# Optimization experiments

Hardware: AMD Instinct MI355X
Metric: run time of the kernel (lower is better)

The kernel has to match this reference:

```python
import jax, jax.numpy as jnp
import numpy as np

EPS = 1e-8
LAMBDA_SOFTMAX = 9.0
LAMBDA_LSE = 6.0
MARGIN = 0.2


def setup_inputs() -> dict:
    key = jax.random.key(0)
    k1, k2, k3 = jax.random.split(key, 3)
    B, R, W, D = 128, 36, 64, 1024
    im = jax.random.normal(k1, (B, R, D), dtype=jnp.float32)
    s = jax.random.normal(k2, (B, W, D), dtype=jnp.float32)
    s_l = jax.random.randint(k3, (B,), 8, W + 1, dtype=jnp.int32)
    return {"im": im, "s": s, "s_l": s_l}


def _xattn_scores_t2i(im, s, s_l):
    # im: [B, R, D] images; s: [B, W, D] captions; s_l: [B] caption lengths
    B, W = s.shape[0], s.shape[1]
    wmask = (jnp.arange(W)[None, :] < s_l[:, None]).astype(im.dtype)  # [B, W]

    def per_caption(args):
        cap, wm = args  # cap: [W, D], wm: [W]
        # raw attention: context=images, query=caption words -> [B, R, W]
        attn = jnp.einsum('ird,wd->irw', im, cap)
        # clipped_l2norm: leakyrelu(0.1) then l2norm over word dim; padded words zeroed
        attn = jax.nn.leaky_relu(attn, 0.1) * wm
        attn = attn / (jnp.sqrt(jnp.sum(attn * attn, axis=2, keepdims=True)) + EPS)
        # transpose to [B, W, R], softmax over regions with smoothing
        attn = jax.nn.softmax(jnp.swapaxes(attn, 1, 2) * LAMBDA_SOFTMAX, axis=2)
        # weighted image context per word: [B, W, D]
        wei = jnp.einsum('iwr,ird->iwd', attn, im)
        # cosine similarity between caption words and weighted context
        num = jnp.einsum('iwd,wd->iw', wei, cap)
        n_cap = jnp.sqrt(jnp.sum(cap * cap, axis=-1))      # [W]
        n_wei = jnp.sqrt(jnp.sum(wei * wei, axis=-1))      # [B, W]
        row = num / jnp.maximum(n_cap[None, :] * n_wei, EPS)
        # LogSumExp aggregation over valid words -> [B]
        return jnp.log(jnp.sum(jnp.exp(LAMBDA_LSE * row) * wm[None, :], axis=1)) / LAMBDA_LSE

    cols = jax.lax.map(per_caption, (s, wmask))  # [B_cap, B_img]
    return cols.T  # scores[i, j]: image i vs caption j


def reference(im, s, s_l):
    scores = _xattn_scores_t2i(im, s, s_l)  # [B, B]
    B = scores.shape[0]
    diag = jnp.diagonal(scores)[:, None]  # [B, 1]
    cost_s = jnp.clip(MARGIN + scores - diag, 0.0)       # caption retrieval
    cost_im = jnp.clip(MARGIN + scores - diag.T, 0.0)    # image retrieval
    off = 1.0 - jnp.eye(B, dtype=scores.dtype)
    cost_s = cost_s * off
    cost_im = cost_im * off
    # max_violation=True: hardest negatives
    cost_s = jnp.max(cost_s, axis=1)
    cost_im = jnp.max(cost_im, axis=0)
    return jnp.sum(cost_s) + jnp.sum(cost_im)
```

## Files before the change

### kernel.cpp

```cpp
#include <hip/hip_runtime.h>
#include <hip/hip_bf16.h>
#include <math.h>
#include <stdint.h>

#define NB 128
#define NR 36
#define NW 64
#define ND 1024
#define MT 48
#define EPSF 1e-8f
#define LAM_SM 9.0f
#define LAM_LSE 6.0f
#define MARGINF 0.2f

typedef _Float16 f16;
typedef f16 f16x4 __attribute__((ext_vector_type(4)));
typedef f16 f16x8 __attribute__((ext_vector_type(8)));
typedef float f32x4 __attribute__((ext_vector_type(4)));
typedef int i32x4 __attribute__((ext_vector_type(4)));
typedef int i32x8 __attribute__((ext_vector_type(8)));

__device__ __forceinline__ void gld_lds16(const void* g, void* l) {
    __builtin_amdgcn_global_load_lds(
        (const __attribute__((address_space(1))) uint32_t*)(uintptr_t)g,
        (__attribute__((address_space(3))) uint32_t*)(uint32_t)(uintptr_t)l,
        16, 0, 0);
}

__device__ __forceinline__ uint32_t pk_fp8x4(float4 v) {
    uint32_t w = 0;
    w = __builtin_amdgcn_cvt_pk_fp8_f32(v.x, v.y, w, false);
    w = __builtin_amdgcn_cvt_pk_fp8_f32(v.z, v.w, w, true);
    return w;
}

__global__ __launch_bounds__(256) void prep_kernel(
    const float* __restrict__ im, const float* __restrict__ s,
    uint8_t* __restrict__ im8, uint8_t* __restrict__ s8, float* __restrict__ ncap,
    f16* __restrict__ Mg16) {
    __shared__ __align__(16) char Gs[8192];
    const int b = blockIdx.x, y = blockIdx.y, t = threadIdx.x;

    if (y < 14) {
        const int lr = t >> 5, g = t & 31;
        const int row = y * 8 + lr;
        if (row < MT) {
            uint32_t* dst = (uint32_t*)(im8 + ((size_t)b * MT + row) * ND);
            if (row < NR) {
                const float4* src = (const float4*)(im + ((size_t)b * NR + row) * ND);
                #pragma unroll
                for (int e = 0; e < 8; ++e)
                    dst[g + e * 32] = pk_fp8x4(src[g + e * 32]);
            } else {
                #pragma unroll
                for (int e = 0; e < 8; ++e) dst[g + e * 32] = 0u;
            }
        } else {
            const int w = row - MT;
            const float4* src = (const float4*)(s + ((size_t)b * NW + w) * ND);
            uint32_t* dst = (uint32_t*)(s8 + ((size_t)b * NW + w) * ND);
            float ss = 0.f;
            #pragma unroll
            for (int e = 0; e < 8; ++e) {
                float4 v = src[g + e * 32];
                dst[g + e * 32] = pk_fp8x4(v);
                ss += v.x * v.x + v.y * v.y + v.z * v.z + v.w * v.w;
            }
            #pragma unroll
            for (int off = 1; off < 32; off <<= 1) ss += __shfl_xor(ss, off, 32);
            if (g == 0) ncap[b * NW + w] = sqrtf(ss);
        }
        return;
    }

    const int wave = t >> 6, lane = t & 63;
    const int quad = lane >> 4, l16 = lane & 15;
    const int nt = wave;
    f32x4 acc[3];
    acc[0] = (f32x4){0.f, 0.f, 0.f, 0.f};
    acc[1] = (f32x4){0.f, 0.f, 0.f, 0.f};
    acc[2] = (f32x4){0.f, 0.f, 0.f, 0.f};
    const float* imb = im + (size_t)b * NR * ND;

    for (int kk = 0; kk < ND; kk += 64) {
        for (int cidx = t; cidx < 512; cidx += 256) {
            int row = cidx >> 3, c = cidx & 7;
            f16x8 hv;
            if (row < NR) {
                const float4* sp = (const float4*)(imb + (size_t)row * ND + kk + c * 8);
                float4 v0 = sp[0], v1 = sp[1];
                hv = (f16x8){(f16)v0.x, (f16)v0.y, (f16)v0.z, (f16)v0.w,
                             (f16)v1.x, (f16)v1.y, (f16)v1.z, (f16)v1.w};
            } else {
                hv = (f16x8){(f16)0.f, (f16)0.f, (f16)0.f, (f16)0.f,
                             (f16)0.f, (f16)0.f, (f16)0.f, (f16)0.f};
            }
            *(f16x8*)(Gs + row * 128 + ((c ^ (row & 7)) * 16)) = hv;
        }
        __syncthreads();
        #pragma unroll
        for (int ks = 0; ks < 2; ++ks) {
            int brow = nt * 16 + l16;
            f16x8 bf = *(const f16x8*)(Gs + brow * 128 + (((ks * 4 + quad) ^ (brow & 7)) * 16));
            #pragma unroll
            for (int mt = 0; mt < 3; ++mt) {
                int arow = mt * 16 + l16;
                f16x8 af = *(const f16x8*)(Gs + arow * 128 + (((ks * 4 + quad) ^ (arow & 7)) * 16));
                acc[mt] = __builtin_amdgcn_mfma_f32_16x16x32_f16(af, bf, acc[mt], 0, 0, 0);
            }
        }
        __syncthreads();
    }
    f16* Mb = Mg16 + (size_t)b * (MT * NW);
    #pragma unroll
    for (int mt = 0; mt < 3; ++mt) {
        #pragma unroll
        for (int r = 0; r < 4; ++r) {
            int row = mt * 16 + quad * 4 + r;
            Mb[row * NW + nt * 16 + l16] = (f16)acc[mt][r];
        }
    }
}

#define A_LDS 12288
__global__ __launch_bounds__(256) void fused_pair_kernel(
    const uint8_t* __restrict__ im8, const uint8_t* __restrict__ s8,
    const int* __restrict__ s_l, const f16* __restrict__ Mg16,
    const float* __restrict__ ncap, float* __restrict__ scores) {
    __shared__ __align__(16) char lds[32768];
    const int t = threadIdx.x;
    const int wave = t >> 6, lane = t & 63;
    const int quad = lane >> 4, l16 = lane & 15;
    const int wi = wave >> 1, wj = wave & 1;

    const int lin = blockIdx.x;
    const int gx = lin & 63, gy = lin >> 6;
    const int i = gy * 2 + wi;
    const int j = gx * 2 + wj;
    const int L = s_l[j];

    const uint8_t* Ab = im8 + (size_t)gy * 2 * (MT * ND);
    const uint8_t* Bb = s8 + (size_t)gx * 2 * (NW * ND);

    int goff[7];
    bool gact[7];
    const uint8_t* gbase[7];
    #pragma unroll
    for (int q = 0; q < 7; ++q) {
        int f = q * 4096 + t * 16;
        if (f < A_LDS) {
            int row = f >> 7, c = (f >> 4) & 7;
            goff[q] = row * ND + (c ^ (row & 7)) * 16;
            gact[q] = (row % MT) < NR;
            gbase[q] = Ab;
        } else {
            int f2 = f - A_LDS;
            int row = f2 >> 7, c = (f2 >> 4) & 7;
            goff[q] = row * ND + (c ^ (row & 7)) * 16;
            gact[q] = true;
            gbase[q] = Bb;
        }
    }

    if (t < 192) {
        int r = (t < 96) ? (36 + (t >> 3)) : (84 + ((t - 96) >> 3));
        *(float4*)(lds + r * 128 + (t & 7) * 16) = make_float4(0.f, 0.f, 0.f, 0.f);
    }

    f32x4 acc[3][4];
    #pragma unroll
    for (int mi = 0; mi < 3; ++mi)
        #pragma unroll
        for (int nt = 0; nt < 4; ++nt)
            acc[mi][nt] = (f32x4){0.f, 0.f, 0.f, 0.f};

    const int c0 = quad * 2, c1 = quad * 2 + 1;

    for (int kk = 0; kk < ND; kk += 128) {
        #pragma unroll
        for (int q = 0; q < 7; ++q)
            if (gact[q]) gld_lds16(gbase[q] + goff[q] + kk, lds + q * 4096 + t * 16);
        __syncthreads();
        i32x8 bf[4];
        #pragma unroll
        for (int nt = 0; nt < 4; ++nt) {
            int row = wj * 64 + nt * 16 + l16;
            const char* base = lds + A_LDS + row * 128;
            i32x4 lo = *(const i32x4*)(base + ((c0 ^ (row & 7)) * 16));
            i32x4 hi = *(const i32x4*)(base + ((c1 ^ (row & 7)) * 16));
            bf[nt] = (i32x8){lo.x, lo.y, lo.z, lo.w, hi.x, hi.y, hi.z, hi.w};
        }
        #pragma unroll
        for (int mi = 0; mi < 3; ++mi) {
            int row = wi * 48 + mi * 16 + l16;
            const char* base = lds + row * 128;
            i32x4 lo = *(const i32x4*)(base + ((c0 ^ (row & 7)) * 16));
            i32x4 hi = *(const i32x4*)(base + ((c1 ^ (row & 7)) * 16));
            i32x8 af = (i32x8){lo.x, lo.y, lo.z, lo.w, hi.x, hi.y, hi.z, hi.w};
            #pragma unroll
            for (int nt = 0; nt < 4; ++nt)
                acc[mi][nt] = __builtin_amdgcn_mfma_scale_f32_16x16x128_f8f6f4(
                    af, bf[nt], acc[mi][nt], 0, 0, 0, 0x7F, 0, 0x7F);
        }
        __syncthreads();
    }

    char* waveE = lds + wave * 8192;
    {
        int col = lane;
        f16x8 z = {(f16)0.f,(f16)0.f,(f16)0.f,(f16)0.f,(f16)0.f,(f16)0.f,(f16)0.f,(f16)0.f};
        *(f16x8*)(waveE + col * 128 + ((6 ^ (col & 7)) * 16)) = z;
        *(f16x8*)(waveE + col * 128 + ((7 ^ (col & 7)) * 16)) = z;
    }

    float rn[3][4];
    #pragma unroll
    for (int mi = 0; mi < 3; ++mi) {
        #pragma unroll
        for (int r = 0; r < 4; ++r) {
            int row = mi * 16 + quad * 4 + r;
            float ss = 0.f;
            #pragma unroll
            for (int nt = 0; nt < 4; ++nt) {
                int col = nt * 16 + l16;
                float v = acc[mi][nt][r];
                float lv = v > 0.f ? v : 0.1f * v;
                if (col < L) ss += lv * lv;
            }
            ss += __shfl_xor(ss, 1, 64);
            ss += __shfl_xor(ss, 2, 64);
            ss += __shfl_xor(ss, 4, 64);
            ss += __shfl_xor(ss, 8, 64);
            rn[mi][r] = (row < NR) ? 1.0f / (sqrtf(ss) + EPSF) : 0.f;
        }
    }
    float cs[4] = {0.f, 0.f, 0.f, 0.f}, nu[4] = {0.f, 0.f, 0.f, 0.f};
    #pragma unroll
    for (int mi = 0; mi < 3; ++mi) {
        #pragma unroll
        for (int nt = 0; nt < 4; ++nt) {
            int col = nt * 16 + l16;
            f16x4 ew;
            #pragma unroll
            for (int r = 0; r < 4; ++r) {
                float v = acc[mi][nt][r];
                float lv = v > 0.f ? v : 0.1f * v;
                float e = __expf(LAM_SM * ((col < L) ? lv * rn[mi][r] : 0.f));
                ew[r] = (f16)e;
                if (mi * 16 + quad * 4 + r < NR) { cs[nt] += e; nu[nt] += e * v; }
            }
            int c = mi * 2 + (quad >> 1);
            *(f16x4*)(waveE + col * 128 + ((c ^ (col & 7)) * 16) + (quad & 1) * 8) = ew;
        }
    }
    #pragma unroll
    for (int nt = 0; nt < 4; ++nt) {
        cs[nt] += __shfl_xor(cs[nt], 16, 64); cs[nt] += __shfl_xor(cs[nt], 32, 64);
        nu[nt] += __shfl_xor(nu[nt], 16, 64); nu[nt] += __shfl_xor(nu[nt], 32, 64);
    }

    const f16* Mi = Mg16 + (size_t)i * (MT * NW);
    float qf[4] = {0.f, 0.f, 0.f, 0.f};
    #pragma unroll
    for (int mi = 0; mi < 3; ++mi) {
        f32x4 y[4];
        #pragma unroll
        for (int nt = 0; nt < 4; ++nt) y[nt] = (f32x4){0.f, 0.f, 0.f, 0.f};
        #pragma unroll
        for (int ks = 0; ks < 2; ++ks) {
            f16x8 aq = *(const f16x8*)(Mi + (mi * 16 + l16) * NW + ks * 32 + quad * 8);
            #pragma unroll
            for (int nt = 0; nt < 4; ++nt) {
                int col = nt * 16 + l16;
                int pch = (ks * 4 + quad) ^ (col & 7);
                f16x8 bq = *(const f16x8*)(waveE + col * 128 + pch * 16);
                y[nt] = __builtin_amdgcn_mfma_f32_16x16x32_f16(aq, bq, y[nt], 0, 0, 0);
            }
        }
        int row0 = mi * 16 + quad * 4;
        int c = row0 >> 3, sub = (row0 >> 2) & 1;
        #pragma unroll
        for (int nt = 0; nt < 4; ++nt) {
            int col = nt * 16 + l16;
            f16x4 ev = *(const f16x4*)(waveE + col * 128 + ((c ^ (col & 7)) * 16) + sub * 8);
            #pragma unroll
            for (int r = 0; r < 4; ++r) qf[nt] += y[nt][r] * (float)ev[r];
        }
    }
    #pragma unroll
    for (int nt = 0; nt < 4; ++nt) {
        qf[nt] += __shfl_xor(qf[nt], 16, 64); qf[nt] += __shfl_xor(qf[nt], 32, 64);
    }
    float lse = 0.f;
    #pragma unroll
    for (int nt = 0; nt < 4; ++nt) {
        int col = nt * 16 + l16;
        float num  = nu[nt] / cs[nt];
        float nwei = sqrtf(fmaxf(qf[nt], 0.f)) / cs[nt];
        float nc   = ncap[j * NW + col];
        float rowv = num / fmaxf(nc * nwei, EPSF);
        lse += (col < L) ? __expf(LAM_LSE * rowv) : 0.f;
    }
    lse += __shfl_xor(lse, 1, 64);
    lse += __shfl_xor(lse, 2, 64);
    lse += __shfl_xor(lse, 4, 64);
    lse += __shfl_xor(lse, 8, 64);
    if (lane == 0) scores[i * NB + j] = __logf(lse) / LAM_LSE;
}

__global__ __launch_bounds__(256) void loss_kernel(const float* __restrict__ S,
                                                   float* __restrict__ out) {
    __shared__ __align__(16) float Sl[NB * NB];
    __shared__ float part[NB];
    __shared__ float wsum[2];
    int t = threadIdx.x;
    for (int c = t; c < (NB * NB) / 4; c += 256)
        ((float4*)Sl)[c] = ((const float4*)S)[c];
    __syncthreads();
    if (t < NB) {
        float dii = Sl[t * NB + t];
        float rmax = 0.f, cmax = 0.f;
        for (int k = 0; k < NB; ++k) {
            if (k != t) {
                float vs = MARGINF + Sl[t * NB + k] - dii;
                rmax = fmaxf(rmax, fmaxf(vs, 0.f));
                float vi = MARGINF + Sl[k * NB + t] - dii;
                cmax = fmaxf(cmax, fmaxf(vi, 0.f));
            }
        }
        part[t] = rmax + cmax;
    }
    __syncthreads();
    if (t < NB) {
        float v = part[t];
        #pragma unroll
        for (int off = 1; off < 64; off <<= 1) v += __shfl_xor(v, off, 64);
        if ((t & 63) == 0) wsum[t >> 6] = v;
    }
    __syncthreads();
    if (t == 0) out[0] = wsum[0] + wsum[1];
}

extern "C" void kernel_launch(void* const* d_in, const int* in_sizes, int n_in,
                              void* d_out, int out_size, void* d_ws, size_t ws_size,
                              hipStream_t stream) {
    const float* im  = (const float*)d_in[0];
    const float* s   = (const float*)d_in[1];
    const int*   s_l = (const int*)d_in[2];

    float*   scores = (float*)d_ws;
    float*   ncap   = scores + NB * NB;
    f16*     Mg16   = (f16*)(ncap + NB * NW);
    uint8_t* im8    = (uint8_t*)(Mg16 + (size_t)NB * MT * NW);
    uint8_t* s8     = im8 + (size_t)NB * MT * ND;

    dim3 pgrid(NB, 15);
    prep_kernel<<<pgrid, 256, 0, stream>>>(im, s, im8, s8, ncap, Mg16);
    fused_pair_kernel<<<4096, 256, 0, stream>>>(im8, s8, s_l, Mg16, ncap, scores);
    loss_kernel<<<1, 256, 0, stream>>>(scores, (float*)d_out);
}
```

Measured before the change: 229.4 us.

## Double-buffer LDS staging in fused pair kernel K-loop

Replaces the single-buffered K loop in the fused pair kernel with a double-buffered pipeline. The global-to-LDS loads for the next K chunk are issued before the MFMA work on the current chunk, and one barrier per iteration is removed. It also precomputes swizzled LDS offsets, fully unrolls the loop and adds a min-blocks hint of 2 to launch_bounds. In exchange LDS use nearly doubles to 56 KB per block, which may limit occupancy, and register pressure goes up.

```diff
diff --git a/kernel.cpp b/kernel.cpp
--- a/kernel.cpp
+++ b/kernel.cpp
@@ -123,11 +123,12 @@
 }
 
 #define A_LDS 12288
-__global__ __launch_bounds__(256) void fused_pair_kernel(
+#define STG   28672
+__global__ __launch_bounds__(256, 2) void fused_pair_kernel(
     const uint8_t* __restrict__ im8, const uint8_t* __restrict__ s8,
     const int* __restrict__ s_l, const f16* __restrict__ Mg16,
     const float* __restrict__ ncap, float* __restrict__ scores) {
-    __shared__ __align__(16) char lds[32768];
+    __shared__ __align__(16) char lds[2 * STG];
     const int t = threadIdx.x;
     const int wave = t >> 6, lane = t & 63;
     const int quad = lane >> 4, l16 = lane & 15;
@@ -165,6 +166,7 @@
     if (t < 192) {
         int r = (t < 96) ? (36 + (t >> 3)) : (84 + ((t - 96) >> 3));
         *(float4*)(lds + r * 128 + (t & 7) * 16) = make_float4(0.f, 0.f, 0.f, 0.f);
+        *(float4*)(lds + STG + r * 128 + (t & 7) * 16) = make_float4(0.f, 0.f, 0.f, 0.f);
     }
 
     f32x4 acc[3][4];
@@ -176,32 +178,57 @@
 
     const int c0 = quad * 2, c1 = quad * 2 + 1;
 
-    for (int kk = 0; kk < ND; kk += 128) {
-        #pragma unroll
-        for (int q = 0; q < 7; ++q)
-            if (gact[q]) gld_lds16(gbase[q] + goff[q] + kk, lds + q * 4096 + t * 16);
-        __syncthreads();
-        i32x8 bf[4];
+    int boff0[4], boff1[4];
+    #pragma unroll
+    for (int nt = 0; nt < 4; ++nt) {
+        int row = wj * 64 + nt * 16 + l16;
+        int base = A_LDS + row * 128;
+        boff0[nt] = base + ((c0 ^ (row & 7)) * 16);
+        boff1[nt] = base + ((c1 ^ (row & 7)) * 16);
+    }
+    int aoff0[3], aoff1[3];
+    #pragma unroll
+    for (int mi = 0; mi < 3; ++mi) {
+        int row = wi * 48 + mi * 16 + l16;
+        int base = row * 128;
+        aoff0[mi] = base + ((c0 ^ (row & 7)) * 16);
+        aoff1[mi] = base + ((c1 ^ (row & 7)) * 16);
+    }
+
+    #pragma unroll
+    for (int q = 0; q < 7; ++q)
+        if (gact[q]) gld_lds16(gbase[q] + goff[q], lds + q * 4096 + t * 16);
+    __syncthreads();
+
+    #pragma unroll
+    for (int it = 0; it < 8; ++it) {
+        const int cb = (it & 1) ? STG : 0;
+        if (it < 7) {
+            const int nb = (it & 1) ? 0 : STG;
+            const int kk = (it + 1) * 128;
+            #pragma unroll
+            for (int q = 0; q < 7; ++q)
+                if (gact[q]) gld_lds16(gbase[q] + goff[q] + kk, lds + nb + q * 4096 + t * 16);
+        }
+        i32x8 bf[4], af[3];
         #pragma unroll
         for (int nt = 0; nt < 4; ++nt) {
-            int row = wj * 64 + nt * 16 + l16;
-            const char* base = lds + A_LDS + row * 128;
-            i32x4 lo = *(const i32x4*)(base + ((c0 ^ (row & 7)) * 16));
-            i32x4 hi = *(const i32x4*)(base + ((c1 ^ (row & 7)) * 16));
+            i32x4 lo = *(const i32x4*)(lds + cb + boff0[nt]);
+            i32x4 hi = *(const i32x4*)(lds + cb + boff1[nt]);
             bf[nt] = (i32x8){lo.x, lo.y, lo.z, lo.w, hi.x, hi.y, hi.z, hi.w};
         }
         #pragma unroll
         for (int mi = 0; mi < 3; ++mi) {
-            int row = wi * 48 + mi * 16 + l16;
-            const char* base = lds + row * 128;
-            i32x4 lo = *(const i32x4*)(base + ((c0 ^ (row & 7)) * 16));
-            i32x4 hi = *(const i32x4*)(base + ((c1 ^ (row & 7)) * 16));
-            i32x8 af = (i32x8){lo.x, lo.y, lo.z, lo.w, hi.x, hi.y, hi.z, hi.w};
+            i32x4 lo = *(const i32x4*)(lds + cb + aoff0[mi]);
+            i32x4 hi = *(const i32x4*)(lds + cb + aoff1[mi]);
+            af[mi] = (i32x8){lo.x, lo.y, lo.z, lo.w, hi.x, hi.y, hi.z, hi.w};
+        }
+        #pragma unroll
+        for (int mi = 0; mi < 3; ++mi)
             #pragma unroll
             for (int nt = 0; nt < 4; ++nt)
                 acc[mi][nt] = __builtin_amdgcn_mfma_scale_f32_16x16x128_f8f6f4(
-                    af, bf[nt], acc[mi][nt], 0, 0, 0, 0x7F, 0, 0x7F);
-        }
+                    af[mi], bf[nt], acc[mi][nt], 0, 0, 0, 0x7F, 0, 0x7F);
         __syncthreads();
     }
 
```

After: 343.0 us. 1.5x slower.

## Pre-swizzle fp8 operands into MFMA fragment order and load directly from global

Applied to the files above, without the earlier changes.

The prep kernel now writes fp8 image and caption data in a per-k-chunk, per-16-row tile layout matching the MFMA lane fragment order. The main GEMM loop then loads each wave's A and B fragments straight from global memory as 32-byte vectors, with no LDS staging and no block barriers. This removes the shared-memory staging, swizzle math and syncthreads. In exchange, the four waves of a block no longer share loaded tiles and each wave depends on L2/cache for reuse, with less latency hiding.

```diff
diff --git a/kernel.cpp b/kernel.cpp
--- a/kernel.cpp
+++ b/kernel.cpp
@@ -20,19 +20,13 @@
 typedef int i32x4 __attribute__((ext_vector_type(4)));
 typedef int i32x8 __attribute__((ext_vector_type(8)));
 
-__device__ __forceinline__ void gld_lds16(const void* g, void* l) {
-    __builtin_amdgcn_global_load_lds(
-        (const __attribute__((address_space(1))) uint32_t*)(uintptr_t)g,
-        (__attribute__((address_space(3))) uint32_t*)(uint32_t)(uintptr_t)l,
-        16, 0, 0);
-}
-
 __device__ __forceinline__ uint32_t pk_fp8x4(float4 v) {
     uint32_t w = 0;
     w = __builtin_amdgcn_cvt_pk_fp8_f32(v.x, v.y, w, false);
     w = __builtin_amdgcn_cvt_pk_fp8_f32(v.z, v.w, w, true);
     return w;
 }
+
 
 __global__ __launch_bounds__(256) void prep_kernel(
     const float* __restrict__ im, const float* __restrict__ s,
@@ -45,25 +39,42 @@
         const int lr = t >> 5, g = t & 31;
         const int row = y * 8 + lr;
         if (row < MT) {
-            uint32_t* dst = (uint32_t*)(im8 + ((size_t)b * MT + row) * ND);
+            const int mi = row >> 4, l16 = row & 15;
+            uint32_t* dstd = (uint32_t*)im8;
             if (row < NR) {
                 const float4* src = (const float4*)(im + ((size_t)b * NR + row) * ND);
                 #pragma unroll
-                for (int e = 0; e < 8; ++e)
-                    dst[g + e * 32] = pk_fp8x4(src[g + e * 32]);
+                for (int e = 0; e < 8; ++e) {
+                    int di = g + e * 32;
+                    int kc = di >> 5, q = (di >> 3) & 3, bw = di & 7;
+                    size_t dst = ((size_t)(b * 8 + kc) * 3 + mi) * 512
+                                 + (q * 16 + l16) * 8 + bw;
+                    dstd[dst] = pk_fp8x4(src[di]);
+                }
             } else {
                 #pragma unroll
-                for (int e = 0; e < 8; ++e) dst[g + e * 32] = 0u;
+                for (int e = 0; e < 8; ++e) {
+                    int di = g + e * 32;
+                    int kc = di >> 5, q = (di >> 3) & 3, bw = di & 7;
+                    size_t dst = ((size_t)(b * 8 + kc) * 3 + mi) * 512
+                                 + (q * 16 + l16) * 8 + bw;
+                    dstd[dst] = 0u;
+                }
             }
         } else {
             const int w = row - MT;
+            const int nt = w >> 4, l16 = w & 15;
             const float4* src = (const float4*)(s + ((size_t)b * NW + w) * ND);
-            uint32_t* dst = (uint32_t*)(s8 + ((size_t)b * NW + w) * ND);
+            uint32_t* dstd = (uint32_t*)s8;
             float ss = 0.f;
             #pragma unroll
             for (int e = 0; e < 8; ++e) {
-                float4 v = src[g + e * 32];
-                dst[g + e * 32] = pk_fp8x4(v);
+                int di = g + e * 32;
+                int kc = di >> 5, q = (di >> 3) & 3, bw = di & 7;
+                float4 v = src[di];
+                size_t dst = ((size_t)(b * 8 + kc) * 4 + nt) * 512
+                             + (q * 16 + l16) * 8 + bw;
+                dstd[dst] = pk_fp8x4(v);
                 ss += v.x * v.x + v.y * v.y + v.z * v.z + v.w * v.w;
             }
             #pragma unroll
@@ -122,7 +133,6 @@
     }
 }
 
-#define A_LDS 12288
 __global__ __launch_bounds__(256) void fused_pair_kernel(
     const uint8_t* __restrict__ im8, const uint8_t* __restrict__ s8,
     const int* __restrict__ s_l, const f16* __restrict__ Mg16,
@@ -139,34 +149,6 @@
     const int j = gx * 2 + wj;
     const int L = s_l[j];
 
-    const uint8_t* Ab = im8 + (size_t)gy * 2 * (MT * ND);
-    const uint8_t* Bb = s8 + (size_t)gx * 2 * (NW * ND);
-
-    int goff[7];
-    bool gact[7];
-    const uint8_t* gbase[7];
-    #pragma unroll
-    for (int q = 0; q < 7; ++q) {
-        int f = q * 4096 + t * 16;
-        if (f < A_LDS) {
-            int row = f >> 7, c = (f >> 4) & 7;
-            goff[q] = row * ND + (c ^ (row & 7)) * 16;
-            gact[q] = (row % MT) < NR;
-            gbase[q] = Ab;
-        } else {
-            int f2 = f - A_LDS;
-            int row = f2 >> 7, c = (f2 >> 4) & 7;
-            goff[q] = row * ND + (c ^ (row & 7)) * 16;
-            gact[q] = true;
-            gbase[q] = Bb;
-        }
-    }
-
-    if (t < 192) {
-        int r = (t < 96) ? (36 + (t >> 3)) : (84 + ((t - 96) >> 3));
-        *(float4*)(lds + r * 128 + (t & 7) * 16) = make_float4(0.f, 0.f, 0.f, 0.f);
-    }
-
     f32x4 acc[3][4];
     #pragma unroll
     for (int mi = 0; mi < 3; ++mi)
@@ -174,35 +156,25 @@
         for (int nt = 0; nt < 4; ++nt)
             acc[mi][nt] = (f32x4){0.f, 0.f, 0.f, 0.f};
 
-    const int c0 = quad * 2, c1 = quad * 2 + 1;
-
-    for (int kk = 0; kk < ND; kk += 128) {
-        #pragma unroll
-        for (int q = 0; q < 7; ++q)
-            if (gact[q]) gld_lds16(gbase[q] + goff[q] + kk, lds + q * 4096 + t * 16);
-        __syncthreads();
+    const uint8_t* Afrag = im8 + (size_t)i * (8 * 3 * 2048) + lane * 32;
+    const uint8_t* Bfrag = s8 + (size_t)j * (8 * 4 * 2048) + lane * 32;
+
+    #pragma unroll 1
+    for (int kc = 0; kc < 8; ++kc) {
+        const uint8_t* Ak = Afrag + (size_t)kc * (3 * 2048);
+        const uint8_t* Bk = Bfrag + (size_t)kc * (4 * 2048);
         i32x8 bf[4];
         #pragma unroll
-        for (int nt = 0; nt < 4; ++nt) {
-            int row = wj * 64 + nt * 16 + l16;
-            const char* base = lds + A_LDS + row * 128;
-            i32x4 lo = *(const i32x4*)(base + ((c0 ^ (row & 7)) * 16));
-            i32x4 hi = *(const i32x4*)(base + ((c1 ^ (row & 7)) * 16));
-            bf[nt] = (i32x8){lo.x, lo.y, lo.z, lo.w, hi.x, hi.y, hi.z, hi.w};
-        }
+        for (int nt = 0; nt < 4; ++nt)
+            bf[nt] = *(const i32x8*)(Bk + nt * 2048);
         #pragma unroll
         for (int mi = 0; mi < 3; ++mi) {
-            int row = wi * 48 + mi * 16 + l16;
-            const char* base = lds + row * 128;
-            i32x4 lo = *(const i32x4*)(base + ((c0 ^ (row & 7)) * 16));
-            i32x4 hi = *(const i32x4*)(base + ((c1 ^ (row & 7)) * 16));
-            i32x8 af = (i32x8){lo.x, lo.y, lo.z, lo.w, hi.x, hi.y, hi.z, hi.w};
+            i32x8 af = *(const i32x8*)(Ak + mi * 2048);
             #pragma unroll
             for (int nt = 0; nt < 4; ++nt)
                 acc[mi][nt] = __builtin_amdgcn_mfma_scale_f32_16x16x128_f8f6f4(
                     af, bf[nt], acc[mi][nt], 0, 0, 0, 0x7F, 0, 0x7F);
         }
-        __syncthreads();
     }
 
     char* waveE = lds + wave * 8192;
```

New measurement: 212.0 us. -7.6%, faster.
